# Kernel tuning notes

Hardware: AMD Instinct MI355X
Metric: run time of the kernel (lower is better)

## Reference

```python
import jax, jax.numpy as jnp
import numpy as np

IN_DIM, H, OUT_DIM = 64, 128, 64
B, T = 1024, 512
NEG_SLOPE = 0.01
LN_EPS = 1e-5


def _mlp_layer(x, W, b, g, beta):
    h = x @ W.T + b
    h = jnp.where(h > 0, h, NEG_SLOPE * h)  # LeakyReLU
    mu = h.mean(-1, keepdims=True)
    var = h.var(-1, keepdims=True)
    return g * (h - mu) / jnp.sqrt(var + LN_EPS) + beta


def setup_inputs() -> dict:
    key = jax.random.key(0)
    ks = jax.random.split(key, 16)
    s = 1.0 / np.sqrt(H)
    return {
        "x": jax.random.normal(ks[0], (B, T, IN_DIM), jnp.float32),
        "is_init": jax.random.randint(ks[1], (B, T, 1), 0, 2) > 0,
        "hx": jax.random.normal(ks[2], (B, H), jnp.float32),
        "W1": jax.random.uniform(ks[3], (H, IN_DIM), jnp.float32, -s, s),
        "b1": jnp.zeros((H,), jnp.float32),
        "g1": jnp.ones((H,), jnp.float32),
        "beta1": jnp.zeros((H,), jnp.float32),
        "W2": jax.random.uniform(ks[4], (H, H), jnp.float32, -s, s),
        "b2": jnp.zeros((H,), jnp.float32),
        "g2": jnp.ones((H,), jnp.float32),
        "beta2": jnp.zeros((H,), jnp.float32),
        "W_ih": jax.random.uniform(ks[5], (3 * H, H), jnp.float32, -s, s),
        "W_hh": jax.random.uniform(ks[6], (3 * H, H), jnp.float32, -s, s),
        "b_ih": jax.random.uniform(ks[7], (3 * H,), jnp.float32, -s, s),
        "b_hh": jax.random.uniform(ks[8], (3 * H,), jnp.float32, -s, s),
        "W_out": jax.random.uniform(ks[9], (OUT_DIM, H), jnp.float32, -s, s),
        "b_out": jnp.zeros((OUT_DIM,), jnp.float32),
    }


def reference(x, is_init, hx, W1, b1, g1, beta1, W2, b2, g2, beta2,
              W_ih, W_hh, b_ih, b_hh, W_out, b_out):
    # MLP: two (Linear -> LeakyReLU -> LayerNorm) layers, width 128
    h = _mlp_layer(x, W1, b1, g1, beta1)
    h = _mlp_layer(h, W2, b2, g2, beta2)

    # Precompute input-side gate preactivations for all timesteps: [B,T,3H]
    gates_x = h @ W_ih.T + b_ih
    gates_x_t = jnp.swapaxes(gates_x, 0, 1)      # [T,B,3H]
    init_t = jnp.swapaxes(is_init, 0, 1)         # [T,B,1]

    def step(h_prev, inp):
        gx, init = inp
        h_prev = jnp.where(init, 0.0, h_prev)    # reset-on-init
        gh = h_prev @ W_hh.T + b_hh
        xr, xz, xn = jnp.split(gx, 3, axis=-1)
        hr, hz, hn = jnp.split(gh, 3, axis=-1)
        r = jax.nn.sigmoid(xr + hr)
        z = jax.nn.sigmoid(xz + hz)
        n = jnp.tanh(xn + r * hn)
        h_new = (1.0 - z) * n + z * h_prev
        return h_new, h_new

    hx_final, ys = jax.lax.scan(step, hx, (gates_x_t, init_t))
    y = jnp.swapaxes(ys, 0, 1)                   # [B,T,H]
    out = y @ W_out.T + b_out                    # [B,T,OUT_DIM]
    return out, hx_final
```

## Files before the change

kernel.cpp:

```cpp
#include <hip/hip_runtime.h>
#include <hip/hip_bf16.h>

#define IN_DIM 64
#define H 128
#define G3 384
#define OUT_DIM 64
#define Bb 1024
#define Tt 512
#define NEG 0.01f
#define EPSLN 1e-5f

#define CHUNK 16
#define NCHUNK (Tt / CHUNK)

typedef __bf16 bf16_t;
typedef __bf16 bf16x8 __attribute__((ext_vector_type(8)));
typedef float f32x4 __attribute__((ext_vector_type(4)));

#define GX_OFF 0
#define GXS 392
#define HA_OFF 50176
#define HAS 136
#define HPF_OFF 67584
#define HPB_OFF 69632
#define RED_OFF 73984
#define MNR_OFF 76032
#define GHB_OFF 76544
#define GHS 388
#define VEC_OFF 82752
#define INI_OFF 89152
#define SMEM_BYTES 89440

#define V_B1 0
#define V_G1 128
#define V_BE1 256
#define V_B2 384
#define V_G2 512
#define V_BE2 640
#define V_BIH 768
#define V_BHH 1152
#define V_BOUT 1536

#define MFMA(a, b, c) __builtin_amdgcn_mfma_f32_16x16x32_bf16((a), (b), (c), 0, 0, 0)

__global__ void __launch_bounds__(256, 1) gru_fused(
    const float* __restrict__ x, const int* __restrict__ is_init,
    const float* __restrict__ hx,
    const float* __restrict__ W1, const float* __restrict__ b1,
    const float* __restrict__ g1, const float* __restrict__ be1,
    const float* __restrict__ W2, const float* __restrict__ b2,
    const float* __restrict__ g2, const float* __restrict__ be2,
    const float* __restrict__ Wih, const float* __restrict__ Whh,
    const float* __restrict__ bih, const float* __restrict__ bhh,
    const float* __restrict__ Wout, const float* __restrict__ bout,
    float* __restrict__ out)
{
    extern __shared__ char smem[];
    bf16_t* GX  = (bf16_t*)(smem + GX_OFF);
    bf16_t* HA  = (bf16_t*)(smem + HA_OFF);
    float*  HPF = (float*) (smem + HPF_OFF);
    bf16_t* HPB = (bf16_t*)(smem + HPB_OFF);
    float*  RED = (float*) (smem + RED_OFF);
    float*  MNR = (float*) (smem + MNR_OFF);
    float*  GHB = (float*) (smem + GHB_OFF);
    float*  VEC = (float*) (smem + VEC_OFF);
    int*    INI = (int*)   (smem + INI_OFF);

    const int tid  = threadIdx.x;
    const int w    = tid >> 6;
    const int lane = tid & 63;
    const int ln   = lane & 15;
    const int quad = lane >> 4;
    const int b0   = blockIdx.x * 4;

    for (int i = tid; i < H; i += 256) {
        VEC[V_B1 + i] = b1[i];  VEC[V_G1 + i] = g1[i];  VEC[V_BE1 + i] = be1[i];
        VEC[V_B2 + i] = b2[i];  VEC[V_G2 + i] = g2[i];  VEC[V_BE2 + i] = be2[i];
    }
    for (int i = tid; i < G3; i += 256) {
        VEC[V_BIH + i] = bih[i];  VEC[V_BHH + i] = bhh[i];
    }
    if (tid < OUT_DIM) VEC[V_BOUT + tid] = bout[tid];
    for (int i = tid; i < 16 * HAS; i += 256) HPB[i] = (bf16_t)0.f;
    __syncthreads();
    for (int job = tid; job < 512; job += 256) {
        int b = job >> 7, j = job & 127;
        int im = is_init[(size_t)(b0 + b) * Tt];
        float v = im ? 0.f : hx[(size_t)(b0 + b) * H + j];
        HPF[b * H + j] = v;
        HPB[b * HAS + j] = (bf16_t)v;
    }
    bf16x8 whhf[6][4];
#pragma unroll
    for (int ntl = 0; ntl < 6; ++ntl) {
        int gate = ntl >> 1, sub = ntl & 1;
        int n = gate * H + w * 32 + sub * 16 + ln;
        const float* p = Whh + (size_t)n * H;
#pragma unroll
        for (int ks = 0; ks < 4; ++ks) {
            const float* q = p + ks * 32 + quad * 8;
            bf16x8 f;
#pragma unroll
            for (int j = 0; j < 8; ++j) f[j] = (bf16_t)q[j];
            whhf[ntl][ks] = f;
        }
    }
    __syncthreads();

    for (int tc = 0; tc < NCHUNK; ++tc) {
        const int t0 = tc * CHUNK;

        f32x4 vs[4][2];

        {
            bf16x8 w1f[2][2];
#pragma unroll
            for (int ntl = 0; ntl < 2; ++ntl) {
                int n = w * 32 + ntl * 16 + ln;
                const float* p = W1 + (size_t)n * IN_DIM;
#pragma unroll
                for (int ks = 0; ks < 2; ++ks) {
                    const float* q = p + ks * 32 + quad * 8;
                    bf16x8 f;
#pragma unroll
                    for (int j = 0; j < 8; ++j) f[j] = (bf16_t)q[j];
                    w1f[ntl][ks] = f;
                }
            }
#pragma unroll
            for (int mt = 0; mt < 4; ++mt) {
                const float* xr_ = x + ((size_t)(b0 + mt) * Tt + t0 + ln) * IN_DIM;
                bf16x8 a0, a1;
#pragma unroll
                for (int j = 0; j < 8; ++j) {
                    a0[j] = (bf16_t)xr_[quad * 8 + j];
                    a1[j] = (bf16_t)xr_[32 + quad * 8 + j];
                }
#pragma unroll
                for (int ntl = 0; ntl < 2; ++ntl) {
                    f32x4 c = {0.f, 0.f, 0.f, 0.f};
                    c = MFMA(a0, w1f[ntl][0], c);
                    c = MFMA(a1, w1f[ntl][1], c);
                    vs[mt][ntl] = c;
                }
            }
            float bv[2], gv[2], bev[2];
#pragma unroll
            for (int ntl = 0; ntl < 2; ++ntl) {
                int n = w * 32 + ntl * 16 + ln;
                bv[ntl] = VEC[V_B1 + n]; gv[ntl] = VEC[V_G1 + n]; bev[ntl] = VEC[V_BE1 + n];
            }
#pragma unroll
            for (int mt = 0; mt < 4; ++mt) {
#pragma unroll
                for (int reg = 0; reg < 4; ++reg) {
                    float v0 = vs[mt][0][reg] + bv[0]; v0 = v0 > 0.f ? v0 : NEG * v0;
                    float v1 = vs[mt][1][reg] + bv[1]; v1 = v1 > 0.f ? v1 : NEG * v1;
                    vs[mt][0][reg] = v0; vs[mt][1][reg] = v1;
                    float s = v0 + v1, q = v0 * v0 + v1 * v1;
#pragma unroll
                    for (int d = 1; d < 16; d <<= 1) { s += __shfl_xor(s, d); q += __shfl_xor(q, d); }
                    if (ln == 0) {
                        int rr = mt * 16 + quad * 4 + reg;
                        RED[rr * 8 + w] = s; RED[rr * 8 + 4 + w] = q;
                    }
                }
            }
            __syncthreads();
            if (tid < 64) {
                float s = RED[tid * 8] + RED[tid * 8 + 1] + RED[tid * 8 + 2] + RED[tid * 8 + 3];
                float q = RED[tid * 8 + 4] + RED[tid * 8 + 5] + RED[tid * 8 + 6] + RED[tid * 8 + 7];
                float mean = s * (1.f / H);
                float var = q * (1.f / H) - mean * mean;
                MNR[tid * 2] = mean; MNR[tid * 2 + 1] = rsqrtf(var + EPSLN);
            }
            __syncthreads();
#pragma unroll
            for (int mt = 0; mt < 4; ++mt) {
#pragma unroll
                for (int reg = 0; reg < 4; ++reg) {
                    int rr = mt * 16 + quad * 4 + reg;
                    float mean = MNR[rr * 2], rstd = MNR[rr * 2 + 1];
#pragma unroll
                    for (int ntl = 0; ntl < 2; ++ntl) {
                        int n = w * 32 + ntl * 16 + ln;
                        HA[rr * HAS + n] = (bf16_t)(gv[ntl] * (vs[mt][ntl][reg] - mean) * rstd + bev[ntl]);
                    }
                }
            }
            __syncthreads();
        }

        {
            bf16x8 w2f[2][4];
#pragma unroll
            for (int ntl = 0; ntl < 2; ++ntl) {
                int n = w * 32 + ntl * 16 + ln;
                const float* p = W2 + (size_t)n * H;
#pragma unroll
                for (int ks = 0; ks < 4; ++ks) {
                    const float* q = p + ks * 32 + quad * 8;
                    bf16x8 f;
#pragma unroll
                    for (int j = 0; j < 8; ++j) f[j] = (bf16_t)q[j];
                    w2f[ntl][ks] = f;
                }
            }
#pragma unroll
            for (int mt = 0; mt < 4; ++mt) {
                bf16x8 af[4];
#pragma unroll
                for (int ks = 0; ks < 4; ++ks)
                    af[ks] = *(const bf16x8*)(HA + (mt * 16 + ln) * HAS + ks * 32 + quad * 8);
#pragma unroll
                for (int ntl = 0; ntl < 2; ++ntl) {
                    f32x4 c = {0.f, 0.f, 0.f, 0.f};
#pragma unroll
                    for (int ks = 0; ks < 4; ++ks) c = MFMA(af[ks], w2f[ntl][ks], c);
                    vs[mt][ntl] = c;
                }
            }
            float bv[2], gv[2], bev[2];
#pragma unroll
            for (int ntl = 0; ntl < 2; ++ntl) {
                int n = w * 32 + ntl * 16 + ln;
                bv[ntl] = VEC[V_B2 + n]; gv[ntl] = VEC[V_G2 + n]; bev[ntl] = VEC[V_BE2 + n];
            }
#pragma unroll
            for (int mt = 0; mt < 4; ++mt) {
#pragma unroll
                for (int reg = 0; reg < 4; ++reg) {
                    float v0 = vs[mt][0][reg] + bv[0]; v0 = v0 > 0.f ? v0 : NEG * v0;
                    float v1 = vs[mt][1][reg] + bv[1]; v1 = v1 > 0.f ? v1 : NEG * v1;
                    vs[mt][0][reg] = v0; vs[mt][1][reg] = v1;
                    float s = v0 + v1, q = v0 * v0 + v1 * v1;
#pragma unroll
                    for (int d = 1; d < 16; d <<= 1) { s += __shfl_xor(s, d); q += __shfl_xor(q, d); }
                    if (ln == 0) {
                        int rr = mt * 16 + quad * 4 + reg;
                        RED[rr * 8 + w] = s; RED[rr * 8 + 4 + w] = q;
                    }
                }
            }
            __syncthreads();
            if (tid < 64) {
                float s = RED[tid * 8] + RED[tid * 8 + 1] + RED[tid * 8 + 2] + RED[tid * 8 + 3];
                float q = RED[tid * 8 + 4] + RED[tid * 8 + 5] + RED[tid * 8 + 6] + RED[tid * 8 + 7];
                float mean = s * (1.f / H);
                float var = q * (1.f / H) - mean * mean;
                MNR[tid * 2] = mean; MNR[tid * 2 + 1] = rsqrtf(var + EPSLN);
            }
            __syncthreads();
#pragma unroll
            for (int mt = 0; mt < 4; ++mt) {
#pragma unroll
                for (int reg = 0; reg < 4; ++reg) {
                    int rr = mt * 16 + quad * 4 + reg;
                    float mean = MNR[rr * 2], rstd = MNR[rr * 2 + 1];
#pragma unroll
                    for (int ntl = 0; ntl < 2; ++ntl) {
                        int n = w * 32 + ntl * 16 + ln;
                        HA[rr * HAS + n] = (bf16_t)(gv[ntl] * (vs[mt][ntl][reg] - mean) * rstd + bev[ntl]);
                    }
                }
            }
            __syncthreads();
        }

        for (int ntl = 0; ntl < 6; ++ntl) {
            int n = (w * 6 + ntl) * 16 + ln;
            const float* p = Wih + (size_t)n * H;
            bf16x8 bf[4];
#pragma unroll
            for (int ks = 0; ks < 4; ++ks) {
                const float* q = p + ks * 32 + quad * 8;
                bf16x8 f;
#pragma unroll
                for (int j = 0; j < 8; ++j) f[j] = (bf16_t)q[j];
                bf[ks] = f;
            }
            float bv = VEC[V_BIH + n];
#pragma unroll
            for (int mt = 0; mt < 4; ++mt) {
                bf16x8 af[4];
#pragma unroll
                for (int ks = 0; ks < 4; ++ks)
                    af[ks] = *(const bf16x8*)(HA + (mt * 16 + ln) * HAS + ks * 32 + quad * 8);
                f32x4 c = {0.f, 0.f, 0.f, 0.f};
#pragma unroll
                for (int ks = 0; ks < 4; ++ks) c = MFMA(af[ks], bf[ks], c);
#pragma unroll
                for (int reg = 0; reg < 4; ++reg)
                    GX[(mt * 16 + quad * 4 + reg) * GXS + n] = (bf16_t)(c[reg] + bv);
            }
        }
        if (tid < 68) {
            int b = tid / 17, s = tid % 17;
            int t = t0 + s;
            INI[tid] = (t < Tt) ? is_init[(size_t)(b0 + b) * Tt + t] : 0;
        }

        for (int s = 0; s < CHUNK; ++s) {
            __syncthreads();
            bf16x8 af[4];
#pragma unroll
            for (int ks = 0; ks < 4; ++ks)
                af[ks] = *(const bf16x8*)(HPB + ln * HAS + ks * 32 + quad * 8);
            f32x4 gc[6];
#pragma unroll
            for (int ntl = 0; ntl < 6; ++ntl) {
                f32x4 c = {0.f, 0.f, 0.f, 0.f};
#pragma unroll
                for (int ks = 0; ks < 4; ++ks) c = MFMA(af[ks], whhf[ntl][ks], c);
                gc[ntl] = c;
            }
            if (quad == 0) {
#pragma unroll
                for (int ntl = 0; ntl < 6; ++ntl) {
                    int gate = ntl >> 1, sub = ntl & 1;
                    int n = gate * H + w * 32 + sub * 16 + ln;
#pragma unroll
                    for (int reg = 0; reg < 4; ++reg)
                        GHB[reg * GHS + n] = gc[ntl][reg];
                }
            }
            __syncthreads();
            const int t = t0 + s;
#pragma unroll
            for (int rep = 0; rep < 2; ++rep) {
                int job = tid + rep * 256;
                int b = job >> 7, j = job & 127;
                int rrow = b * 16 + s;
                float xr = (float)GX[rrow * GXS + j];
                float xz = (float)GX[rrow * GXS + H + j];
                float xn = (float)GX[rrow * GXS + 2 * H + j];
                float hr = GHB[b * GHS + j]         + VEC[V_BHH + j];
                float hz = GHB[b * GHS + H + j]     + VEC[V_BHH + H + j];
                float hn = GHB[b * GHS + 2 * H + j] + VEC[V_BHH + 2 * H + j];
                float r = 1.f / (1.f + __expf(-(xr + hr)));
                float z = 1.f / (1.f + __expf(-(xz + hz)));
                float a = xn + r * hn;
                a = fminf(fmaxf(a, -15.f), 15.f);
                float e = __expf(-2.f * a);
                float nn = (1.f - e) / (1.f + e);
                float hp = HPF[b * H + j];
                float hnew = (1.f - z) * nn + z * hp;
                HA[rrow * HAS + j] = (bf16_t)hnew;
                float hm;
                if (t < Tt - 1) {
                    hm = INI[b * 17 + s + 1] ? 0.f : hnew;
                } else {
                    hm = hnew;
                    out[(size_t)Bb * Tt * OUT_DIM + (size_t)(b0 + b) * H + j] = hnew;
                }
                HPF[b * H + j] = hm;
                HPB[b * HAS + j] = (bf16_t)hm;
            }
        }
        __syncthreads();

        {
            int o = w * 16 + ln;
            const float* p = Wout + (size_t)o * H;
            bf16x8 wof[4];
#pragma unroll
            for (int ks = 0; ks < 4; ++ks) {
                const float* q = p + ks * 32 + quad * 8;
                bf16x8 f;
#pragma unroll
                for (int j = 0; j < 8; ++j) f[j] = (bf16_t)q[j];
                wof[ks] = f;
            }
            float bo = VEC[V_BOUT + o];
#pragma unroll
            for (int mt = 0; mt < 4; ++mt) {
                bf16x8 af[4];
#pragma unroll
                for (int ks = 0; ks < 4; ++ks)
                    af[ks] = *(const bf16x8*)(HA + (mt * 16 + ln) * HAS + ks * 32 + quad * 8);
                f32x4 c = {0.f, 0.f, 0.f, 0.f};
#pragma unroll
                for (int ks = 0; ks < 4; ++ks) c = MFMA(af[ks], wof[ks], c);
#pragma unroll
                for (int reg = 0; reg < 4; ++reg)
                    out[((size_t)(b0 + mt) * Tt + t0 + quad * 4 + reg) * OUT_DIM + o] = c[reg] + bo;
            }
        }
        __syncthreads();
    }
}

extern "C" void kernel_launch(void* const* d_in, const int* in_sizes, int n_in,
                              void* d_out, int out_size, void* d_ws, size_t ws_size,
                              hipStream_t stream) {
    const float* x      = (const float*)d_in[0];
    const int*   is_init= (const int*)  d_in[1];
    const float* hx     = (const float*)d_in[2];
    const float* W1     = (const float*)d_in[3];
    const float* b1     = (const float*)d_in[4];
    const float* g1     = (const float*)d_in[5];
    const float* be1    = (const float*)d_in[6];
    const float* W2     = (const float*)d_in[7];
    const float* b2     = (const float*)d_in[8];
    const float* g2     = (const float*)d_in[9];
    const float* be2    = (const float*)d_in[10];
    const float* Wih    = (const float*)d_in[11];
    const float* Whh    = (const float*)d_in[12];
    const float* bih    = (const float*)d_in[13];
    const float* bhh    = (const float*)d_in[14];
    const float* Wout   = (const float*)d_in[15];
    const float* bout   = (const float*)d_in[16];
    float* out = (float*)d_out;

    hipFuncSetAttribute((const void*)gru_fused,
                        hipFuncAttributeMaxDynamicSharedMemorySize, SMEM_BYTES);
    gru_fused<<<Bb / 4, 256, SMEM_BYTES, stream>>>(
        x, is_init, hx, W1, b1, g1, be1, W2, b2, g2, be2,
        Wih, Whh, bih, bhh, Wout, bout, out);
}
```

Measured before the change: 1.548 ms.

## Halve batch per block, keep GRU gates in registers, double-buffer hidden state

Each block now processes 2 batch rows instead of 4, which doubles the grid and shrinks shared memory so two blocks can fit per CU (launch bounds raised to 2). The recurrent step computes the gate nonlinearities directly from MFMA accumulators held in registers in quad-0 lanes, instead of staging them through a shared GHB buffer. The hidden state is kept in registers and written to a ping-pong shared buffer, which removes one barrier per timestep. The x loads are also vectorised. In exchange, only a quarter of the lanes do the elementwise gate work, and with 2 rows the 16-row MFMA tiles are mostly padding, so matrix-unit work per useful row rises.

```diff
diff --git a/kernel.cpp b/kernel.cpp
--- a/kernel.cpp
+++ b/kernel.cpp
@@ -12,6 +12,7 @@
 
 #define CHUNK 16
 #define NCHUNK (Tt / CHUNK)
+#define ROWS 32
 
 typedef __bf16 bf16_t;
 typedef __bf16 bf16x8 __attribute__((ext_vector_type(8)));
@@ -19,17 +20,15 @@
 
 #define GX_OFF 0
 #define GXS 392
-#define HA_OFF 50176
+#define HA_OFF 25088
 #define HAS 136
-#define HPF_OFF 67584
-#define HPB_OFF 69632
-#define RED_OFF 73984
-#define MNR_OFF 76032
-#define GHB_OFF 76544
-#define GHS 388
-#define VEC_OFF 82752
-#define INI_OFF 89152
-#define SMEM_BYTES 89440
+#define HPB_OFF 33792
+#define HPB_STRIDE 2176
+#define RED_OFF 42496
+#define MNR_OFF 43520
+#define VEC_OFF 43776
+#define INI_OFF 50176
+#define SMEM_BYTES 50368
 
 #define V_B1 0
 #define V_G1 128
@@ -43,7 +42,7 @@
 
 #define MFMA(a, b, c) __builtin_amdgcn_mfma_f32_16x16x32_bf16((a), (b), (c), 0, 0, 0)
 
-__global__ void __launch_bounds__(256, 1) gru_fused(
+__global__ void __launch_bounds__(256, 2) gru_fused(
     const float* __restrict__ x, const int* __restrict__ is_init,
     const float* __restrict__ hx,
     const float* __restrict__ W1, const float* __restrict__ b1,
@@ -58,11 +57,9 @@
     extern __shared__ char smem[];
     bf16_t* GX  = (bf16_t*)(smem + GX_OFF);
     bf16_t* HA  = (bf16_t*)(smem + HA_OFF);
-    float*  HPF = (float*) (smem + HPF_OFF);
     bf16_t* HPB = (bf16_t*)(smem + HPB_OFF);
     float*  RED = (float*) (smem + RED_OFF);
     float*  MNR = (float*) (smem + MNR_OFF);
-    float*  GHB = (float*) (smem + GHB_OFF);
     float*  VEC = (float*) (smem + VEC_OFF);
     int*    INI = (int*)   (smem + INI_OFF);
 
@@ -71,7 +68,7 @@
     const int lane = tid & 63;
     const int ln   = lane & 15;
     const int quad = lane >> 4;
-    const int b0   = blockIdx.x * 4;
+    const int b0   = blockIdx.x * 2;
 
     for (int i = tid; i < H; i += 256) {
         VEC[V_B1 + i] = b1[i];  VEC[V_G1 + i] = g1[i];  VEC[V_BE1 + i] = be1[i];
@@ -81,15 +78,28 @@
         VEC[V_BIH + i] = bih[i];  VEC[V_BHH + i] = bhh[i];
     }
     if (tid < OUT_DIM) VEC[V_BOUT + tid] = bout[tid];
-    for (int i = tid; i < 16 * HAS; i += 256) HPB[i] = (bf16_t)0.f;
+    for (int i = tid; i < 2 * HPB_STRIDE; i += 256) HPB[i] = (bf16_t)0.f;
     __syncthreads();
-    for (int job = tid; job < 512; job += 256) {
-        int b = job >> 7, j = job & 127;
-        int im = is_init[(size_t)(b0 + b) * Tt];
-        float v = im ? 0.f : hx[(size_t)(b0 + b) * H + j];
-        HPF[b * H + j] = v;
-        HPB[b * HAS + j] = (bf16_t)v;
+
+    float hpr[2][2];
+    float bhr[2], bhz[2], bhn[2];
+    if (quad == 0) {
+#pragma unroll
+        for (int sub = 0; sub < 2; ++sub) {
+            int j = w * 32 + sub * 16 + ln;
+            bhr[sub] = VEC[V_BHH + j];
+            bhz[sub] = VEC[V_BHH + H + j];
+            bhn[sub] = VEC[V_BHH + 2 * H + j];
+#pragma unroll
+            for (int b = 0; b < 2; ++b) {
+                int im = is_init[(size_t)(b0 + b) * Tt];
+                float v = im ? 0.f : hx[(size_t)(b0 + b) * H + j];
+                hpr[sub][b] = v;
+                HPB[b * HAS + j] = (bf16_t)v;
+            }
+        }
     }
+
     bf16x8 whhf[6][4];
 #pragma unroll
     for (int ntl = 0; ntl < 6; ++ntl) {
@@ -107,20 +117,21 @@
     }
     __syncthreads();
 
+    int p = 0;
+
     for (int tc = 0; tc < NCHUNK; ++tc) {
         const int t0 = tc * CHUNK;
-
-        f32x4 vs[4][2];
+        f32x4 vs[2][2];
 
         {
             bf16x8 w1f[2][2];
 #pragma unroll
             for (int ntl = 0; ntl < 2; ++ntl) {
                 int n = w * 32 + ntl * 16 + ln;
-                const float* p = W1 + (size_t)n * IN_DIM;
+                const float* pw = W1 + (size_t)n * IN_DIM;
 #pragma unroll
                 for (int ks = 0; ks < 2; ++ks) {
-                    const float* q = p + ks * 32 + quad * 8;
+                    const float* q = pw + ks * 32 + quad * 8;
                     bf16x8 f;
 #pragma unroll
                     for (int j = 0; j < 8; ++j) f[j] = (bf16_t)q[j];
@@ -128,13 +139,17 @@
                 }
             }
 #pragma unroll
-            for (int mt = 0; mt < 4; ++mt) {
+            for (int mt = 0; mt < 2; ++mt) {
                 const float* xr_ = x + ((size_t)(b0 + mt) * Tt + t0 + ln) * IN_DIM;
+                f32x4 x0 = *(const f32x4*)(xr_ + quad * 8);
+                f32x4 x1 = *(const f32x4*)(xr_ + quad * 8 + 4);
+                f32x4 x2 = *(const f32x4*)(xr_ + 32 + quad * 8);
+                f32x4 x3 = *(const f32x4*)(xr_ + 32 + quad * 8 + 4);
                 bf16x8 a0, a1;
 #pragma unroll
-                for (int j = 0; j < 8; ++j) {
-                    a0[j] = (bf16_t)xr_[quad * 8 + j];
-                    a1[j] = (bf16_t)xr_[32 + quad * 8 + j];
+                for (int j = 0; j < 4; ++j) {
+                    a0[j] = (bf16_t)x0[j]; a0[4 + j] = (bf16_t)x1[j];
+                    a1[j] = (bf16_t)x2[j]; a1[4 + j] = (bf16_t)x3[j];
                 }
 #pragma unroll
                 for (int ntl = 0; ntl < 2; ++ntl) {
@@ -151,7 +166,7 @@
                 bv[ntl] = VEC[V_B1 + n]; gv[ntl] = VEC[V_G1 + n]; bev[ntl] = VEC[V_BE1 + n];
             }
 #pragma unroll
-            for (int mt = 0; mt < 4; ++mt) {
+            for (int mt = 0; mt < 2; ++mt) {
 #pragma unroll
                 for (int reg = 0; reg < 4; ++reg) {
                     float v0 = vs[mt][0][reg] + bv[0]; v0 = v0 > 0.f ? v0 : NEG * v0;
@@ -167,7 +182,7 @@
                 }
             }
             __syncthreads();
-            if (tid < 64) {
+            if (tid < ROWS) {
                 float s = RED[tid * 8] + RED[tid * 8 + 1] + RED[tid * 8 + 2] + RED[tid * 8 + 3];
                 float q = RED[tid * 8 + 4] + RED[tid * 8 + 5] + RED[tid * 8 + 6] + RED[tid * 8 + 7];
                 float mean = s * (1.f / H);
@@ -176,7 +191,7 @@
             }
             __syncthreads();
 #pragma unroll
-            for (int mt = 0; mt < 4; ++mt) {
+            for (int mt = 0; mt < 2; ++mt) {
 #pragma unroll
                 for (int reg = 0; reg < 4; ++reg) {
                     int rr = mt * 16 + quad * 4 + reg;
@@ -196,10 +211,10 @@
 #pragma unroll
             for (int ntl = 0; ntl < 2; ++ntl) {
                 int n = w * 32 + ntl * 16 + ln;
-                const float* p = W2 + (size_t)n * H;
+                const float* pw = W2 + (size_t)n * H;
 #pragma unroll
                 for (int ks = 0; ks < 4; ++ks) {
-                    const float* q = p + ks * 32 + quad * 8;
+                    const float* q = pw + ks * 32 + quad * 8;
                     bf16x8 f;
 #pragma unroll
                     for (int j = 0; j < 8; ++j) f[j] = (bf16_t)q[j];
@@ -207,7 +222,7 @@
                 }
             }
 #pragma unroll
-            for (int mt = 0; mt < 4; ++mt) {
+            for (int mt = 0; mt < 2; ++mt) {
                 bf16x8 af[4];
 #pragma unroll
                 for (int ks = 0; ks < 4; ++ks)
@@ -227,7 +242,7 @@
                 bv[ntl] = VEC[V_B2 + n]; gv[ntl] = VEC[V_G2 + n]; bev[ntl] = VEC[V_BE2 + n];
             }
 #pragma unroll
-            for (int mt = 0; mt < 4; ++mt) {
+            for (int mt = 0; mt < 2; ++mt) {
 #pragma unroll
                 for (int reg = 0; reg < 4; ++reg) {
                     float v0 = vs[mt][0][reg] + bv[0]; v0 = v0 > 0.f ? v0 : NEG * v0;
@@ -243,7 +258,7 @@
                 }
             }
             __syncthreads();
-            if (tid < 64) {
+            if (tid < ROWS) {
                 float s = RED[tid * 8] + RED[tid * 8 + 1] + RED[tid * 8 + 2] + RED[tid * 8 + 3];
                 float q = RED[tid * 8 + 4] + RED[tid * 8 + 5] + RED[tid * 8 + 6] + RED[tid * 8 + 7];
                 float mean = s * (1.f / H);
@@ -252,7 +267,7 @@
             }
             __syncthreads();
 #pragma unroll
-            for (int mt = 0; mt < 4; ++mt) {
+            for (int mt = 0; mt < 2; ++mt) {
 #pragma unroll
                 for (int reg = 0; reg < 4; ++reg) {
                     int rr = mt * 16 + quad * 4 + reg;
@@ -269,11 +284,11 @@
 
         for (int ntl = 0; ntl < 6; ++ntl) {
             int n = (w * 6 + ntl) * 16 + ln;
-            const float* p = Wih + (size_t)n * H;
+            const float* pw = Wih + (size_t)n * H;
             bf16x8 bf[4];
 #pragma unroll
             for (int ks = 0; ks < 4; ++ks) {
-                const float* q = p + ks * 32 + quad * 8;
+                const float* q = pw + ks * 32 + quad * 8;
                 bf16x8 f;
 #pragma unroll
                 for (int j = 0; j < 8; ++j) f[j] = (bf16_t)q[j];
@@ -281,7 +296,7 @@
             }
             float bv = VEC[V_BIH + n];
 #pragma unroll
-            for (int mt = 0; mt < 4; ++mt) {
+            for (int mt = 0; mt < 2; ++mt) {
                 bf16x8 af[4];
 #pragma unroll
                 for (int ks = 0; ks < 4; ++ks)
@@ -294,18 +309,20 @@
                     GX[(mt * 16 + quad * 4 + reg) * GXS + n] = (bf16_t)(c[reg] + bv);
             }
         }
-        if (tid < 68) {
+        if (tid < 34) {
             int b = tid / 17, s = tid % 17;
             int t = t0 + s;
             INI[tid] = (t < Tt) ? is_init[(size_t)(b0 + b) * Tt + t] : 0;
         }
+        __syncthreads();
 
         for (int s = 0; s < CHUNK; ++s) {
-            __syncthreads();
+            bf16_t* Hcur = HPB + p * HPB_STRIDE;
+            bf16_t* Hnxt = HPB + (1 - p) * HPB_STRIDE;
             bf16x8 af[4];
 #pragma unroll
             for (int ks = 0; ks < 4; ++ks)
-                af[ks] = *(const bf16x8*)(HPB + ln * HAS + ks * 32 + quad * 8);
+                af[ks] = *(const bf16x8*)(Hcur + ln * HAS + ks * 32 + quad * 8);
             f32x4 gc[6];
 #pragma unroll
             for (int ntl = 0; ntl < 6; ++ntl) {
@@ -315,57 +332,51 @@
                 gc[ntl] = c;
             }
             if (quad == 0) {
-#pragma unroll
-                for (int ntl = 0; ntl < 6; ++ntl) {
-                    int gate = ntl >> 1, sub = ntl & 1;
-                    int n = gate * H + w * 32 + sub * 16 + ln;
-#pragma unroll
-                    for (int reg = 0; reg < 4; ++reg)
-                        GHB[reg * GHS + n] = gc[ntl][reg];
-                }
-            }
-            __syncthreads();
-            const int t = t0 + s;
-#pragma unroll
-            for (int rep = 0; rep < 2; ++rep) {
-                int job = tid + rep * 256;
-                int b = job >> 7, j = job & 127;
-                int rrow = b * 16 + s;
-                float xr = (float)GX[rrow * GXS + j];
-                float xz = (float)GX[rrow * GXS + H + j];
-                float xn = (float)GX[rrow * GXS + 2 * H + j];
-                float hr = GHB[b * GHS + j]         + VEC[V_BHH + j];
-                float hz = GHB[b * GHS + H + j]     + VEC[V_BHH + H + j];
-                float hn = GHB[b * GHS + 2 * H + j] + VEC[V_BHH + 2 * H + j];
-                float r = 1.f / (1.f + __expf(-(xr + hr)));
-                float z = 1.f / (1.f + __expf(-(xz + hz)));
-                float a = xn + r * hn;
-                a = fminf(fmaxf(a, -15.f), 15.f);
-                float e = __expf(-2.f * a);
-                float nn = (1.f - e) / (1.f + e);
-                float hp = HPF[b * H + j];
-                float hnew = (1.f - z) * nn + z * hp;
-                HA[rrow * HAS + j] = (bf16_t)hnew;
-                float hm;
-                if (t < Tt - 1) {
-                    hm = INI[b * 17 + s + 1] ? 0.f : hnew;
-                } else {
-                    hm = hnew;
-                    out[(size_t)Bb * Tt * OUT_DIM + (size_t)(b0 + b) * H + j] = hnew;
-                }
-                HPF[b * H + j] = hm;
-                HPB[b * HAS + j] = (bf16_t)hm;
-            }
-        }
-        __syncthreads();
+                const int t = t0 + s;
+#pragma unroll
+                for (int sub = 0; sub < 2; ++sub) {
+                    int j = w * 32 + sub * 16 + ln;
+#pragma unroll
+                    for (int b = 0; b < 2; ++b) {
+                        int rr = b * CHUNK + s;
+                        float xr = (float)GX[rr * GXS + j];
+                        float xz = (float)GX[rr * GXS + H + j];
+                        float xn = (float)GX[rr * GXS + 2 * H + j];
+                        float hr = gc[sub][b]     + bhr[sub];
+                        float hz = gc[2 + sub][b] + bhz[sub];
+                        float hn = gc[4 + sub][b] + bhn[sub];
+                        float r = 1.f / (1.f + __expf(-(xr + hr)));
+                        float z = 1.f / (1.f + __expf(-(xz + hz)));
+                        float a = xn + r * hn;
+                        a = fminf(fmaxf(a, -15.f), 15.f);
+                        float e = __expf(-2.f * a);
+                        float nn = (1.f - e) / (1.f + e);
+                        float hp = hpr[sub][b];
+                        float hnew = (1.f - z) * nn + z * hp;
+                        HA[rr * HAS + j] = (bf16_t)hnew;
+                        float hm;
+                        if (t < Tt - 1) {
+                            hm = INI[b * 17 + s + 1] ? 0.f : hnew;
+                        } else {
+                            hm = hnew;
+                            out[(size_t)Bb * Tt * OUT_DIM + (size_t)(b0 + b) * H + j] = hnew;
+                        }
+                        hpr[sub][b] = hm;
+                        Hnxt[b * HAS + j] = (bf16_t)hm;
+                    }
+                }
+            }
+            __syncthreads();
+            p ^= 1;
+        }
 
         {
             int o = w * 16 + ln;
-            const float* p = Wout + (size_t)o * H;
+            const float* pw = Wout + (size_t)o * H;
             bf16x8 wof[4];
 #pragma unroll
             for (int ks = 0; ks < 4; ++ks) {
-                const float* q = p + ks * 32 + quad * 8;
+                const float* q = pw + ks * 32 + quad * 8;
                 bf16x8 f;
 #pragma unroll
                 for (int j = 0; j < 8; ++j) f[j] = (bf16_t)q[j];
@@ -373,7 +384,7 @@
             }
             float bo = VEC[V_BOUT + o];
 #pragma unroll
-            for (int mt = 0; mt < 4; ++mt) {
+            for (int mt = 0; mt < 2; ++mt) {
                 bf16x8 af[4];
 #pragma unroll
                 for (int ks = 0; ks < 4; ++ks)
@@ -414,7 +425,7 @@
 
     hipFuncSetAttribute((const void*)gru_fused,
                         hipFuncAttributeMaxDynamicSharedMemorySize, SMEM_BYTES);
-    gru_fused<<<Bb / 4, 256, SMEM_BYTES, stream>>>(
+    gru_fused<<<Bb / 2, 256, SMEM_BYTES, stream>>>(
         x, is_init, hx, W1, b1, g1, be1, W2, b2, g2, be2,
         Wih, Whh, bih, bhh, Wout, bout, out);
 }
```

After: 1.598 ms. 3.3% more time.
